# Kernel optimization log

Measured on AMD Instinct MI355X. Metric: run time of the kernel, lower is better.

The kernel has to match this reference:

```python
import jax, jax.numpy as jnp
import numpy as np

BLOCK = 32
A16_QMAX = 32767.0  # symmetric 16-bit activation fake-quant
W4_QMAX = 7.0       # symmetric 4-bit per-block weight fake-quant (LPBQ)
EPS = 1e-12


def qdq_a16_per_tensor(x):
    # per-tensor symmetric 16-bit fake quantize / dequantize
    scale = jnp.maximum(jnp.max(jnp.abs(x)) / A16_QMAX, EPS)
    return jnp.clip(jnp.round(x / scale), -A16_QMAX - 1.0, A16_QMAX) * scale


def qdq_weight_lpbq(w):
    # w: [out, in]; block-size-32 groups along the input dim, int4 symmetric
    o, i = w.shape
    wb = w.reshape(o, i // BLOCK, BLOCK)
    scale = jnp.maximum(jnp.max(jnp.abs(wb), axis=-1, keepdims=True) / W4_QMAX, EPS)
    q = jnp.clip(jnp.round(wb / scale), -W4_QMAX - 1.0, W4_QMAX) * scale
    return q.reshape(o, i)


def setup_inputs() -> dict:
    key = jax.random.key(0)
    k0, k1, k2, k3 = jax.random.split(key, 4)
    T, H, I = 4096, 2048, 6144  # tokens, hidden, intermediate
    x = jax.random.normal(k0, (T, H), dtype=jnp.float32)
    w_gate = jax.random.normal(k1, (I, H), dtype=jnp.float32) * 0.02
    w_up = jax.random.normal(k2, (I, H), dtype=jnp.float32) * 0.02
    w_down = jax.random.normal(k3, (H, I), dtype=jnp.float32) * 0.02
    return {"x": x, "w_gate": w_gate, "w_up": w_up, "w_down": w_down}


def reference(x, w_gate, w_up, w_down):
    x = qdq_a16_per_tensor(x)
    up = qdq_a16_per_tensor(x @ qdq_weight_lpbq(w_up).T)      # [T, I]
    gate = qdq_a16_per_tensor(x @ qdq_weight_lpbq(w_gate).T)  # [T, I]
    act = qdq_a16_per_tensor(jax.nn.silu(up))                  # SiLU on up branch (as in source)
    mid = qdq_a16_per_tensor(gate * act)
    return mid @ qdq_weight_lpbq(w_down).T                     # [T, H]
```

## Files before the change

kernel.cpp:

```cpp
#include <hip/hip_runtime.h>

#define T_DIM 4096
#define H_DIM 2048
#define I_DIM 6144

#define BM 128
#define BN 128
#define BK 64

typedef __bf16 bf16x8 __attribute__((ext_vector_type(8)));
typedef float f32x4 __attribute__((ext_vector_type(4)));

__device__ __forceinline__ unsigned short f2bf(float f) {
  unsigned u = __float_as_uint(f);
  u += 0x7FFFu + ((u >> 16) & 1u);
  return (unsigned short)(u >> 16);
}
__device__ __forceinline__ float bf2f(unsigned short h) {
  return __uint_as_float(((unsigned)h) << 16);
}

__device__ __forceinline__ void async16(const unsigned short* g, unsigned short* l) {
  __builtin_amdgcn_global_load_lds(
      (__attribute__((address_space(1))) void*)g,
      (__attribute__((address_space(3))) void*)l, 16, 0, 0);
}

union U8 {
  uint4 v;
  unsigned short h[8];
};

__device__ __forceinline__ void qdq_w_one(const float* __restrict__ w,
                                          unsigned short* __restrict__ out, int i) {
  float4 v = ((const float4*)w)[i];
  float m = fmaxf(fmaxf(fabsf(v.x), fabsf(v.y)), fmaxf(fabsf(v.z), fabsf(v.w)));
  m = fmaxf(m, __shfl_xor(m, 1));
  m = fmaxf(m, __shfl_xor(m, 2));
  m = fmaxf(m, __shfl_xor(m, 4));
  const float s = fmaxf(m * (1.0f / 7.0f), 1e-12f);
  const float inv = 1.0f / s;
  ushort4 o;
  o.x = f2bf(fminf(fmaxf(rintf(v.x * inv), -8.f), 7.f) * s);
  o.y = f2bf(fminf(fmaxf(rintf(v.y * inv), -8.f), 7.f) * s);
  o.z = f2bf(fminf(fmaxf(rintf(v.z * inv), -8.f), 7.f) * s);
  o.w = f2bf(fminf(fmaxf(rintf(v.w * inv), -8.f), 7.f) * s);
  ((ushort4*)out)[i] = o;
}

__global__ void k_prep(const float* __restrict__ x, unsigned short* __restrict__ xq,
                       const float* __restrict__ w0, unsigned short* __restrict__ o0,
                       const float* __restrict__ w1, unsigned short* __restrict__ o1,
                       int nx4, int nw4) {
  const int i = blockIdx.x * blockDim.x + threadIdx.x;
  if (i < nx4) {
    float4 v = ((const float4*)x)[i];
    ushort4 o;
    o.x = f2bf(v.x); o.y = f2bf(v.y); o.z = f2bf(v.z); o.w = f2bf(v.w);
    ((ushort4*)xq)[i] = o;
  } else if (i < nx4 + nw4) {
    qdq_w_one(w0, o0, i - nx4);
  } else {
    qdq_w_one(w1, o1, i - nx4 - nw4);
  }
}

__global__ void k_qdq_w(const float* __restrict__ w, unsigned short* __restrict__ out, int n4) {
  const int i = blockIdx.x * blockDim.x + threadIdx.x;
  if (i < n4) qdq_w_one(w, out, i);
}

template <int LDK>
__device__ __forceinline__ void gemm_core(const unsigned short* __restrict__ A,
                                          const unsigned short* __restrict__ B,
                                          unsigned short* ldsA, unsigned short* ldsB,
                                          long m0, long n0, int tid, f32x4 acc[4][4]) {
  const int lane = tid & 63;
  const int wv = tid >> 6;
  const int wm = (wv >> 1) << 6;
  const int wn = (wv & 1) << 6;
  const int quad = lane >> 4;
  const int l16 = lane & 15;
  const int sw = (l16 & 7);

  for (int k0 = 0; k0 < LDK; k0 += BK) {
    __syncthreads();
#pragma unroll
    for (int r = 0; r < 4; ++r) {
      const int c = r * 256 + tid;
      const int row = c >> 3;
      const int colc = ((c & 7) ^ (row & 7)) * 8;
      async16(A + (m0 + row) * LDK + k0 + colc, ldsA + (size_t)c * 8);
      async16(B + (n0 + row) * LDK + k0 + colc, ldsB + (size_t)c * 8);
    }
    __syncthreads();

#pragma unroll
    for (int ks = 0; ks < BK / 32; ++ks) {
      bf16x8 af[4], bfr[4];
      const int sj = ((ks * 4 + quad) ^ sw) * 8;
#pragma unroll
      for (int i = 0; i < 4; ++i) {
        af[i] = *(const bf16x8*)(ldsA + (wm + i * 16 + l16) * BK + sj);
        bfr[i] = *(const bf16x8*)(ldsB + (wn + i * 16 + l16) * BK + sj);
      }
#pragma unroll
      for (int i = 0; i < 4; ++i)
#pragma unroll
        for (int j = 0; j < 4; ++j)
          acc[i][j] = __builtin_amdgcn_mfma_f32_16x16x32_bf16(af[i], bfr[j], acc[i][j], 0, 0, 0);
    }
  }
}

__launch_bounds__(256)
__global__ void k_gemm_ug(const unsigned short* __restrict__ xq,
                          const unsigned short* __restrict__ wu,
                          const unsigned short* __restrict__ wg,
                          unsigned short* __restrict__ upb,
                          unsigned short* __restrict__ gtb) {
  __shared__ unsigned short lds[(BM + BN) * BK];
  const int tid = threadIdx.x;
  const int NB = I_DIM / BN;
  const bool isUp = (int)blockIdx.x < NB;
  const int bx = isUp ? blockIdx.x : blockIdx.x - NB;
  const unsigned short* B = isUp ? wu : wg;
  unsigned short* C = isUp ? upb : gtb;
  const long m0 = (long)blockIdx.y * BM;
  const long n0 = (long)bx * BN;

  f32x4 acc[4][4] = {};
  gemm_core<H_DIM>(xq, B, lds, lds + BM * BK, m0, n0, tid, acc);

  const int lane = tid & 63;
  const int wv = tid >> 6;
  const int wm = (wv >> 1) << 6;
  const int wn = (wv & 1) << 6;
  const int quad = lane >> 4;
  const int l16 = lane & 15;
  const long rbase = m0 + wm + (quad << 2);
  const long cbase = n0 + wn + l16;
#pragma unroll
  for (int i = 0; i < 4; ++i)
#pragma unroll
    for (int r = 0; r < 4; ++r) {
      const long grow = rbase + i * 16 + r;
#pragma unroll
      for (int j = 0; j < 4; ++j)
        C[grow * (long)I_DIM + cbase + j * 16] = f2bf(acc[i][j][r]);
    }
}

__global__ void k_e1(unsigned short* __restrict__ up, const unsigned short* __restrict__ gt,
                     int n8) {
  const int i = blockIdx.x * blockDim.x + threadIdx.x;
  if (i >= n8) return;
  U8 u, g;
  u.v = ((const uint4*)up)[i];
  g.v = ((const uint4*)gt)[i];
#pragma unroll
  for (int k = 0; k < 8; ++k) {
    const float uv = bf2f(u.h[k]);
    const float a = uv * __frcp_rn(1.0f + __expf(-uv));
    u.h[k] = f2bf(a * bf2f(g.h[k]));
  }
  ((uint4*)up)[i] = u.v;
}

#define DBN 64
__launch_bounds__(256)
__global__ void k_gemm_down(const unsigned short* __restrict__ A,
                            const unsigned short* __restrict__ B,
                            float* __restrict__ C) {
  __shared__ unsigned short lds[(BM + DBN) * BK];
  unsigned short* ldsA = lds;
  unsigned short* ldsB = lds + BM * BK;
  const int tid = threadIdx.x;
  const int lane = tid & 63;
  const int wv = tid >> 6;
  const int wm = (wv >> 1) << 6;
  const int wn = (wv & 1) << 5;
  const int quad = lane >> 4;
  const int l16 = lane & 15;
  const int sw = (l16 & 7);
  const long m0 = (long)blockIdx.y * BM;
  const long n0 = (long)blockIdx.x * DBN;

  f32x4 acc[4][2] = {};

  for (int k0 = 0; k0 < I_DIM; k0 += BK) {
    __syncthreads();
#pragma unroll
    for (int r = 0; r < 4; ++r) {
      const int c = r * 256 + tid;
      const int row = c >> 3;
      const int colc = ((c & 7) ^ (row & 7)) * 8;
      async16(A + (m0 + row) * I_DIM + k0 + colc, ldsA + (size_t)c * 8);
    }
#pragma unroll
    for (int r = 0; r < 2; ++r) {
      const int c = r * 256 + tid;
      const int row = c >> 3;
      const int colc = ((c & 7) ^ (row & 7)) * 8;
      async16(B + (n0 + row) * I_DIM + k0 + colc, ldsB + (size_t)c * 8);
    }
    __syncthreads();

#pragma unroll
    for (int ks = 0; ks < BK / 32; ++ks) {
      bf16x8 af[4], bfr[2];
      const int sj = ((ks * 4 + quad) ^ sw) * 8;
#pragma unroll
      for (int i = 0; i < 4; ++i)
        af[i] = *(const bf16x8*)(ldsA + (wm + i * 16 + l16) * BK + sj);
#pragma unroll
      for (int j = 0; j < 2; ++j)
        bfr[j] = *(const bf16x8*)(ldsB + (wn + j * 16 + l16) * BK + sj);
#pragma unroll
      for (int i = 0; i < 4; ++i)
#pragma unroll
        for (int j = 0; j < 2; ++j)
          acc[i][j] = __builtin_amdgcn_mfma_f32_16x16x32_bf16(af[i], bfr[j], acc[i][j], 0, 0, 0);
    }
  }

  const long rbase = m0 + wm + (quad << 2);
  const long cbase = n0 + wn + l16;
#pragma unroll
  for (int i = 0; i < 4; ++i)
#pragma unroll
    for (int r = 0; r < 4; ++r) {
      const long grow = rbase + i * 16 + r;
#pragma unroll
      for (int j = 0; j < 2; ++j)
        C[grow * (long)H_DIM + cbase + j * 16] = acc[i][j][r];
    }
}

extern "C" void kernel_launch(void* const* d_in, const int* in_sizes, int n_in,
                              void* d_out, int out_size, void* d_ws, size_t ws_size,
                              hipStream_t stream) {
  (void)in_sizes; (void)n_in; (void)out_size; (void)ws_size;
  const float* x      = (const float*)d_in[0];
  const float* w_gate = (const float*)d_in[1];
  const float* w_up   = (const float*)d_in[2];
  const float* w_down = (const float*)d_in[3];

  char* ws = (char*)d_ws;
  const size_t OFF_XQ = 0;
  const size_t OFF_WQ = OFF_XQ + (size_t)T_DIM * H_DIM * 2;
  const size_t OFF_UP = OFF_WQ + (size_t)I_DIM * H_DIM * 2;
  const size_t OFF_GT = OFF_UP + (size_t)T_DIM * I_DIM * 2;
  unsigned short* xq  = (unsigned short*)(ws + OFF_XQ);
  unsigned short* wq  = (unsigned short*)(ws + OFF_WQ);
  unsigned short* upb = (unsigned short*)(ws + OFF_UP);
  unsigned short* gtb = (unsigned short*)(ws + OFF_GT);
  unsigned short* wgq = (unsigned short*)d_out;

  const int nx4 = T_DIM * H_DIM / 4;
  const int nw4 = I_DIM * H_DIM / 4;
  const int ni8 = T_DIM * I_DIM / 8;

  k_prep<<<(nx4 + 2 * nw4) / 256, 256, 0, stream>>>(x, xq, w_up, wq, w_gate, wgq, nx4, nw4);

  k_gemm_ug<<<dim3(2 * I_DIM / BN, T_DIM / BM), 256, 0, stream>>>(xq, wq, wgq, upb, gtb);

  k_qdq_w<<<nw4 / 256, 256, 0, stream>>>(w_down, wq, nw4);

  k_e1<<<ni8 / 256, 256, 0, stream>>>(upb, gtb, ni8);

  k_gemm_down<<<dim3(H_DIM / DBN, T_DIM / BM), 256, 0, stream>>>(upb, wq, (float*)d_out);
}
```

Before: 543.6 us.

## Fuse up/gate GEMMs with SiLU-multiply epilogue and merge weight prep

Each up/gate block now computes both branches against one shared A tile held in LDS. The SiLU(up)*gate product is applied in the epilogue and written as a single bf16 mid tensor. This removes the separate elementwise kernel and the full up and gate intermediate round trips through HBM. The w_down quantization is folded into the prep kernel, and the down GEMM now uses the shared 128x128 gemm_core tile instead of the 128x64 tile. The cost is double the accumulator registers and a larger LDS footprint in the fused kernel, plus fewer blocks in the down GEMM.

```diff
diff --git a/kernel.cpp b/kernel.cpp
--- a/kernel.cpp
+++ b/kernel.cpp
@@ -16,20 +16,12 @@
   u += 0x7FFFu + ((u >> 16) & 1u);
   return (unsigned short)(u >> 16);
 }
-__device__ __forceinline__ float bf2f(unsigned short h) {
-  return __uint_as_float(((unsigned)h) << 16);
-}
 
 __device__ __forceinline__ void async16(const unsigned short* g, unsigned short* l) {
   __builtin_amdgcn_global_load_lds(
       (__attribute__((address_space(1))) void*)g,
       (__attribute__((address_space(3))) void*)l, 16, 0, 0);
 }
-
-union U8 {
-  uint4 v;
-  unsigned short h[8];
-};
 
 __device__ __forceinline__ void qdq_w_one(const float* __restrict__ w,
                                           unsigned short* __restrict__ out, int i) {
@@ -51,6 +43,7 @@
 __global__ void k_prep(const float* __restrict__ x, unsigned short* __restrict__ xq,
                        const float* __restrict__ w0, unsigned short* __restrict__ o0,
                        const float* __restrict__ w1, unsigned short* __restrict__ o1,
+                       const float* __restrict__ w2, unsigned short* __restrict__ o2,
                        int nx4, int nw4) {
   const int i = blockIdx.x * blockDim.x + threadIdx.x;
   if (i < nx4) {
@@ -60,14 +53,11 @@
     ((ushort4*)xq)[i] = o;
   } else if (i < nx4 + nw4) {
     qdq_w_one(w0, o0, i - nx4);
+  } else if (i < nx4 + 2 * nw4) {
+    qdq_w_one(w1, o1, i - nx4 - nw4);
   } else {
-    qdq_w_one(w1, o1, i - nx4 - nw4);
+    qdq_w_one(w2, o2, i - nx4 - 2 * nw4);
   }
-}
-
-__global__ void k_qdq_w(const float* __restrict__ w, unsigned short* __restrict__ out, int n4) {
-  const int i = blockIdx.x * blockDim.x + threadIdx.x;
-  if (i < n4) qdq_w_one(w, out, i);
 }
 
 template <int LDK>
@@ -114,23 +104,89 @@
 }
 
 __launch_bounds__(256)
-__global__ void k_gemm_ug(const unsigned short* __restrict__ xq,
-                          const unsigned short* __restrict__ wu,
-                          const unsigned short* __restrict__ wg,
-                          unsigned short* __restrict__ upb,
-                          unsigned short* __restrict__ gtb) {
+__global__ void k_gemm_ug_fused(const unsigned short* __restrict__ xq,
+                                const unsigned short* __restrict__ wu,
+                                const unsigned short* __restrict__ wg,
+                                unsigned short* __restrict__ mid) {
+  __shared__ unsigned short lds[3 * BM * BK];
+  unsigned short* ldsA = lds;
+  unsigned short* ldsBu = lds + BM * BK;
+  unsigned short* ldsBg = lds + 2 * BM * BK;
+  const int tid = threadIdx.x;
+  const int lane = tid & 63;
+  const int wv = tid >> 6;
+  const int wm = (wv >> 1) << 6;
+  const int wn = (wv & 1) << 6;
+  const int quad = lane >> 4;
+  const int l16 = lane & 15;
+  const int sw = (l16 & 7);
+  const long m0 = (long)blockIdx.y * BM;
+  const long n0 = (long)blockIdx.x * BN;
+
+  f32x4 accU[4][4] = {};
+  f32x4 accG[4][4] = {};
+
+  for (int k0 = 0; k0 < H_DIM; k0 += BK) {
+    __syncthreads();
+#pragma unroll
+    for (int r = 0; r < 4; ++r) {
+      const int c = r * 256 + tid;
+      const int row = c >> 3;
+      const int colc = ((c & 7) ^ (row & 7)) * 8;
+      async16(xq + (m0 + row) * H_DIM + k0 + colc, ldsA + (size_t)c * 8);
+      async16(wu + (n0 + row) * H_DIM + k0 + colc, ldsBu + (size_t)c * 8);
+      async16(wg + (n0 + row) * H_DIM + k0 + colc, ldsBg + (size_t)c * 8);
+    }
+    __syncthreads();
+
+#pragma unroll
+    for (int ks = 0; ks < BK / 32; ++ks) {
+      bf16x8 af[4], bu[4], bg[4];
+      const int sj = ((ks * 4 + quad) ^ sw) * 8;
+#pragma unroll
+      for (int i = 0; i < 4; ++i) {
+        af[i] = *(const bf16x8*)(ldsA + (wm + i * 16 + l16) * BK + sj);
+        bu[i] = *(const bf16x8*)(ldsBu + (wn + i * 16 + l16) * BK + sj);
+        bg[i] = *(const bf16x8*)(ldsBg + (wn + i * 16 + l16) * BK + sj);
+      }
+#pragma unroll
+      for (int i = 0; i < 4; ++i)
+#pragma unroll
+        for (int j = 0; j < 4; ++j) {
+          accU[i][j] = __builtin_amdgcn_mfma_f32_16x16x32_bf16(af[i], bu[j], accU[i][j], 0, 0, 0);
+          accG[i][j] = __builtin_amdgcn_mfma_f32_16x16x32_bf16(af[i], bg[j], accG[i][j], 0, 0, 0);
+        }
+    }
+  }
+
+  const long rbase = m0 + wm + (quad << 2);
+  const long cbase = n0 + wn + l16;
+#pragma unroll
+  for (int i = 0; i < 4; ++i)
+#pragma unroll
+    for (int r = 0; r < 4; ++r) {
+      const long grow = rbase + i * 16 + r;
+#pragma unroll
+      for (int j = 0; j < 4; ++j) {
+        const float u = accU[i][j][r];
+        const float g = accG[i][j][r];
+        const float a = u * __frcp_rn(1.0f + __expf(-u));
+        mid[grow * (long)I_DIM + cbase + j * 16] = f2bf(a * g);
+      }
+    }
+}
+
+__launch_bounds__(256)
+__global__ void k_gemm_down(const unsigned short* __restrict__ A,
+                            const unsigned short* __restrict__ B,
+                            float* __restrict__ C) {
   __shared__ unsigned short lds[(BM + BN) * BK];
   const int tid = threadIdx.x;
-  const int NB = I_DIM / BN;
-  const bool isUp = (int)blockIdx.x < NB;
-  const int bx = isUp ? blockIdx.x : blockIdx.x - NB;
-  const unsigned short* B = isUp ? wu : wg;
-  unsigned short* C = isUp ? upb : gtb;
   const long m0 = (long)blockIdx.y * BM;
-  const long n0 = (long)bx * BN;
+  const long n0 = (long)blockIdx.x * BN;
 
   f32x4 acc[4][4] = {};
-  gemm_core<H_DIM>(xq, B, lds, lds + BM * BK, m0, n0, tid, acc);
+  gemm_core<I_DIM>(A, B, lds, lds + BM * BK, m0, n0, tid, acc);
 
   const int lane = tid & 63;
   const int wv = tid >> 6;
@@ -147,92 +203,6 @@
       const long grow = rbase + i * 16 + r;
 #pragma unroll
       for (int j = 0; j < 4; ++j)
-        C[grow * (long)I_DIM + cbase + j * 16] = f2bf(acc[i][j][r]);
-    }
-}
-
-__global__ void k_e1(unsigned short* __restrict__ up, const unsigned short* __restrict__ gt,
-                     int n8) {
-  const int i = blockIdx.x * blockDim.x + threadIdx.x;
-  if (i >= n8) return;
-  U8 u, g;
-  u.v = ((const uint4*)up)[i];
-  g.v = ((const uint4*)gt)[i];
-#pragma unroll
-  for (int k = 0; k < 8; ++k) {
-    const float uv = bf2f(u.h[k]);
-    const float a = uv * __frcp_rn(1.0f + __expf(-uv));
-    u.h[k] = f2bf(a * bf2f(g.h[k]));
-  }
-  ((uint4*)up)[i] = u.v;
-}
-
-#define DBN 64
-__launch_bounds__(256)
-__global__ void k_gemm_down(const unsigned short* __restrict__ A,
-                            const unsigned short* __restrict__ B,
-                            float* __restrict__ C) {
-  __shared__ unsigned short lds[(BM + DBN) * BK];
-  unsigned short* ldsA = lds;
-  unsigned short* ldsB = lds + BM * BK;
-  const int tid = threadIdx.x;
-  const int lane = tid & 63;
-  const int wv = tid >> 6;
-  const int wm = (wv >> 1) << 6;
-  const int wn = (wv & 1) << 5;
-  const int quad = lane >> 4;
-  const int l16 = lane & 15;
-  const int sw = (l16 & 7);
-  const long m0 = (long)blockIdx.y * BM;
-  const long n0 = (long)blockIdx.x * DBN;
-
-  f32x4 acc[4][2] = {};
-
-  for (int k0 = 0; k0 < I_DIM; k0 += BK) {
-    __syncthreads();
-#pragma unroll
-    for (int r = 0; r < 4; ++r) {
-      const int c = r * 256 + tid;
-      const int row = c >> 3;
-      const int colc = ((c & 7) ^ (row & 7)) * 8;
-      async16(A + (m0 + row) * I_DIM + k0 + colc, ldsA + (size_t)c * 8);
-    }
-#pragma unroll
-    for (int r = 0; r < 2; ++r) {
-      const int c = r * 256 + tid;
-      const int row = c >> 3;
-      const int colc = ((c & 7) ^ (row & 7)) * 8;
-      async16(B + (n0 + row) * I_DIM + k0 + colc, ldsB + (size_t)c * 8);
-    }
-    __syncthreads();
-
-#pragma unroll
-    for (int ks = 0; ks < BK / 32; ++ks) {
-      bf16x8 af[4], bfr[2];
-      const int sj = ((ks * 4 + quad) ^ sw) * 8;
-#pragma unroll
-      for (int i = 0; i < 4; ++i)
-        af[i] = *(const bf16x8*)(ldsA + (wm + i * 16 + l16) * BK + sj);
-#pragma unroll
-      for (int j = 0; j < 2; ++j)
-        bfr[j] = *(const bf16x8*)(ldsB + (wn + j * 16 + l16) * BK + sj);
-#pragma unroll
-      for (int i = 0; i < 4; ++i)
-#pragma unroll
-        for (int j = 0; j < 2; ++j)
-          acc[i][j] = __builtin_amdgcn_mfma_f32_16x16x32_bf16(af[i], bfr[j], acc[i][j], 0, 0, 0);
-    }
-  }
-
-  const long rbase = m0 + wm + (quad << 2);
-  const long cbase = n0 + wn + l16;
-#pragma unroll
-  for (int i = 0; i < 4; ++i)
-#pragma unroll
-    for (int r = 0; r < 4; ++r) {
-      const long grow = rbase + i * 16 + r;
-#pragma unroll
-      for (int j = 0; j < 2; ++j)
         C[grow * (long)H_DIM + cbase + j * 16] = acc[i][j][r];
     }
 }
@@ -248,26 +218,22 @@
 
   char* ws = (char*)d_ws;
   const size_t OFF_XQ = 0;
-  const size_t OFF_WQ = OFF_XQ + (size_t)T_DIM * H_DIM * 2;
-  const size_t OFF_UP = OFF_WQ + (size_t)I_DIM * H_DIM * 2;
-  const size_t OFF_GT = OFF_UP + (size_t)T_DIM * I_DIM * 2;
+  const size_t OFF_WU = OFF_XQ + (size_t)T_DIM * H_DIM * 2;
+  const size_t OFF_WD = OFF_WU + (size_t)I_DIM * H_DIM * 2;
+  const size_t OFF_MID = OFF_WD + (size_t)I_DIM * H_DIM * 2;
   unsigned short* xq  = (unsigned short*)(ws + OFF_XQ);
-  unsigned short* wq  = (unsigned short*)(ws + OFF_WQ);
-  unsigned short* upb = (unsigned short*)(ws + OFF_UP);
-  unsigned short* gtb = (unsigned short*)(ws + OFF_GT);
+  unsigned short* wuq = (unsigned short*)(ws + OFF_WU);
+  unsigned short* wdq = (unsigned short*)(ws + OFF_WD);
+  unsigned short* mid = (unsigned short*)(ws + OFF_MID);
   unsigned short* wgq = (unsigned short*)d_out;
 
   const int nx4 = T_DIM * H_DIM / 4;
   const int nw4 = I_DIM * H_DIM / 4;
-  const int ni8 = T_DIM * I_DIM / 8;
-
-  k_prep<<<(nx4 + 2 * nw4) / 256, 256, 0, stream>>>(x, xq, w_up, wq, w_gate, wgq, nx4, nw4);
-
-  k_gemm_ug<<<dim3(2 * I_DIM / BN, T_DIM / BM), 256, 0, stream>>>(xq, wq, wgq, upb, gtb);
-
-  k_qdq_w<<<nw4 / 256, 256, 0, stream>>>(w_down, wq, nw4);
-
-  k_e1<<<ni8 / 256, 256, 0, stream>>>(upb, gtb, ni8);
-
-  k_gemm_down<<<dim3(H_DIM / DBN, T_DIM / BM), 256, 0, stream>>>(upb, wq, (float*)d_out);
-}
+
+  k_prep<<<(nx4 + 3 * nw4) / 256, 256, 0, stream>>>(x, xq, w_up, wuq, w_gate, wgq,
+                                                    w_down, wdq, nx4, nw4);
+
+  k_gemm_ug_fused<<<dim3(I_DIM / BN, T_DIM / BM), 256, 0, stream>>>(xq, wuq, wgq, mid);
+
+  k_gemm_down<<<dim3(H_DIM / BN, T_DIM / BM), 256, 0, stream>>>(mid, wdq, (float*)d_out);
+}
```

New measurement: 635.6 us. +16.9%, slower.
